# Performance work log

Hardware: AMD Instinct MI355X
Metric: run time of the kernel (lower is better)

Reference implementation:

```python
import jax, jax.numpy as jnp
import numpy as np
import math

B, T, D_MODEL, N_HEADS = 2, 2048, 2048, 16
D_HEAD = D_MODEL // N_HEADS
ROPE_THETA = 10000.0


def setup_inputs() -> dict:
    key = jax.random.key(0)
    ks = jax.random.split(key, 4)
    x = jax.random.normal(ks[0], (B, T, D_MODEL), dtype=jnp.float32)
    # causal mask: True = masked (matches torch masked_fill semantics)
    mask = jnp.triu(jnp.ones((T, T), dtype=bool), k=1)[None, None]  # [1,1,T,T]
    # rotary freqs: complex freqs_cis = exp(i * t * theta^(-2j/d)) -> cos/sin parts
    inv_freq = 1.0 / (ROPE_THETA ** (jnp.arange(0, D_HEAD, 2, dtype=jnp.float32) / D_HEAD))
    angles = jnp.arange(T, dtype=jnp.float32)[:, None] * inv_freq[None, :]  # [T, D_HEAD//2]
    freqs_cos = jnp.cos(angles)
    freqs_sin = jnp.sin(angles)
    s = 1.0 / math.sqrt(D_MODEL)
    Wqkv = jax.random.normal(ks[1], (D_MODEL, 3 * D_MODEL), dtype=jnp.float32) * s
    bqkv = jnp.zeros((3 * D_MODEL,), dtype=jnp.float32)
    Wproj = jax.random.normal(ks[2], (D_MODEL, D_MODEL), dtype=jnp.float32) * s
    bproj = jnp.zeros((D_MODEL,), dtype=jnp.float32)
    return {"x": x, "mask": mask, "freqs_cos": freqs_cos, "freqs_sin": freqs_sin,
            "Wqkv": Wqkv, "bqkv": bqkv, "Wproj": Wproj, "bproj": bproj}


def _rope(t, cos, sin):
    # t: [B,H,T,D]; cos/sin: [1,1,T,D//2]. Complex multiply on (even, odd) pairs.
    t2 = t.reshape(*t.shape[:-1], -1, 2)
    t_re, t_im = t2[..., 0], t2[..., 1]
    out_re = t_re * cos - t_im * sin
    out_im = t_re * sin + t_im * cos
    return jnp.stack([out_re, out_im], axis=-1).reshape(t.shape)


def reference(x, mask, freqs_cos, freqs_sin, Wqkv, bqkv, Wproj, bproj):
    Bb, Tt, C = x.shape
    qkv = x @ Wqkv + bqkv                                   # [B,T,3C]
    q, k, v = jnp.split(qkv, 3, axis=-1)
    def heads(t):
        return t.reshape(Bb, Tt, N_HEADS, D_HEAD).transpose(0, 2, 1, 3)  # [B,H,T,D]
    q, k, v = heads(q), heads(k), heads(v)
    cos = freqs_cos[None, None]                              # [1,1,T,D//2]
    sin = freqs_sin[None, None]
    q = _rope(q, cos, sin)
    k = _rope(k, cos, sin)
    att = jnp.einsum('bhqd,bhkd->bhqk', q, k) / math.sqrt(D_HEAD)
    att = jnp.where(mask, -jnp.inf, att)
    att = jax.nn.softmax(att, axis=-1)
    # attn_dropout is identity in eval mode
    out = jnp.einsum('bhqk,bhkd->bhqd', att, v)              # [B,H,T,D]
    out = out.transpose(0, 2, 1, 3).reshape(Bb, Tt, C)
    return (out @ Wproj + bproj, k, v)
```

## Files before the change

kernel.cpp:

```cpp
#include <hip/hip_runtime.h>
#include <hip/hip_bf16.h>

#define T_SEQ 2048
#define DM    2048
#define NH    16
#define DH    128
#define NBH   32
#define MROWS 4096

typedef __bf16 bf16x8 __attribute__((ext_vector_type(8)));
typedef __bf16 bf16x4 __attribute__((ext_vector_type(4)));
typedef float  f32x4  __attribute__((ext_vector_type(4)));

#define MFMA16 __builtin_amdgcn_mfma_f32_16x16x32_bf16

__device__ __forceinline__ void async_copy16(const void* g, void* l) {
  __builtin_amdgcn_global_load_lds((const __attribute__((address_space(1))) void*)g,
                                   (__attribute__((address_space(3))) void*)l, 16, 0, 0);
}


__global__ void cast_bf16_k(const float* __restrict__ x, __bf16* __restrict__ xb) {
  int i = (blockIdx.x * 256 + threadIdx.x) * 4;
  float4 v = *reinterpret_cast<const float4*>(x + i);
  bf16x4 o;
  o[0] = (__bf16)v.x; o[1] = (__bf16)v.y; o[2] = (__bf16)v.z; o[3] = (__bf16)v.w;
  *reinterpret_cast<bf16x4*>(xb + i) = o;
}

__global__ void transpose_cast_w2(const float* __restrict__ Wqkv, __bf16* __restrict__ WqkvT,
                                  const float* __restrict__ Wproj, __bf16* __restrict__ WprojT) {
  __shared__ float tile[32][33];
  const int bx = (int)blockIdx.x;
  const float* W; __bf16* WT; int N, n0;
  if (bx < 192) { W = Wqkv;  WT = WqkvT;  N = 6144; n0 = bx * 32; }
  else          { W = Wproj; WT = WprojT; N = 2048; n0 = (bx - 192) * 32; }
  const int K = 2048;
  int k0 = blockIdx.y * 32;
  int tx = threadIdx.x, ty = threadIdx.y;
  #pragma unroll
  for (int i = 0; i < 4; i++)
    tile[ty + i * 8][tx] = W[(size_t)(k0 + ty + i * 8) * N + n0 + tx];
  __syncthreads();
  #pragma unroll
  for (int i = 0; i < 4; i++)
    WT[(size_t)(n0 + ty + i * 8) * K + k0 + tx] = (__bf16)tile[tx][ty + i * 8];
}

__global__ void transpose_v(const __bf16* __restrict__ Vb, __bf16* __restrict__ Vtb) {
  __shared__ __bf16 tile[32][34];
  int t0 = blockIdx.x * 32, d0 = blockIdx.y * 32, bh = blockIdx.z;
  const __bf16* src = Vb + (size_t)bh * T_SEQ * DH;
  __bf16* dst = Vtb + (size_t)bh * DH * T_SEQ;
  int tx = threadIdx.x, ty = threadIdx.y;
  #pragma unroll
  for (int i = 0; i < 4; i++)
    tile[ty + i * 8][tx] = src[(size_t)(t0 + ty + i * 8) * DH + d0 + tx];
  __syncthreads();
  #pragma unroll
  for (int i = 0; i < 4; i++)
    dst[(size_t)(d0 + ty + i * 8) * T_SEQ + t0 + tx] = tile[tx][ty + i * 8];
}


__device__ __forceinline__ bf16x8 rds(const __bf16* base, int row, int chunk) {
  return *reinterpret_cast<const bf16x8*>(
      reinterpret_cast<const char*>(base) + row * 128 + ((chunk ^ (row & 7)) << 4));
}

__device__ __forceinline__ void stage64(const __bf16* g, int K, int kt, char* lds,
                                        int wave, int lane) {
  #pragma unroll
  for (int j = 0; j < 4; j++) {
    int r = wave * 32 + j * 8 + (lane >> 3);
    int c = lane & 7;
    const char* src = (const char*)g + (size_t)r * (K * 2) + kt * 128 + ((c ^ (r & 7)) << 4);
    async_copy16(src, lds + wave * 4096 + j * 1024);
  }
}

template <int EPI>
__global__ __launch_bounds__(256, 2) void gemm_bt(
    const __bf16* __restrict__ A, const __bf16* __restrict__ Bt, int K,
    const float* __restrict__ bias,
    const float* __restrict__ fcos, const float* __restrict__ fsin,
    __bf16* __restrict__ Qb, __bf16* __restrict__ Kb, __bf16* __restrict__ Vb,
    float* __restrict__ kout, float* __restrict__ vout,
    float* __restrict__ outp) {
  __shared__ __align__(16) char smem[65536];
  const int tid = threadIdx.x, lane = tid & 63, wave = tid >> 6;
  const int hi = lane >> 4, lo = lane & 15;
  const int wm = (wave >> 1) * 64, wn = (wave & 1) * 64;
  const __bf16* Ab = A + (size_t)blockIdx.y * 128 * K;
  const __bf16* Bb = Bt + (size_t)blockIdx.x * 128 * K;
  f32x4 acc[4][4] = {};
  const int NK = K >> 6;

  stage64(Ab, K, 0, smem, wave, lane);
  stage64(Bb, K, 0, smem + 32768, wave, lane);
  __syncthreads();

  for (int t = 0; t < NK; ++t) {
    const int sel = (t & 1) ? 16384 : 0;
    const __bf16* Ac = (const __bf16*)(smem + sel);
    const __bf16* Bc = (const __bf16*)(smem + 32768 + sel);
    if (t + 1 < NK) {
      stage64(Ab, K, t + 1, smem + (sel ^ 16384), wave, lane);
      stage64(Bb, K, t + 1, smem + 32768 + (sel ^ 16384), wave, lane);
    }
    bf16x8 a0[4], b0[4], a1[4], b1[4];
    #pragma unroll
    for (int m = 0; m < 4; ++m) a0[m] = rds(Ac, wm + m * 16 + lo, hi);
    #pragma unroll
    for (int n = 0; n < 4; ++n) b0[n] = rds(Bc, wn + n * 16 + lo, hi);
    __builtin_amdgcn_s_setprio(1);
    #pragma unroll
    for (int m = 0; m < 4; ++m)
      #pragma unroll
      for (int n = 0; n < 4; ++n)
        acc[m][n] = MFMA16(a0[m], b0[n], acc[m][n], 0, 0, 0);
    __builtin_amdgcn_s_setprio(0);
    #pragma unroll
    for (int m = 0; m < 4; ++m) a1[m] = rds(Ac, wm + m * 16 + lo, 4 + hi);
    #pragma unroll
    for (int n = 0; n < 4; ++n) b1[n] = rds(Bc, wn + n * 16 + lo, 4 + hi);
    __builtin_amdgcn_s_setprio(1);
    #pragma unroll
    for (int m = 0; m < 4; ++m)
      #pragma unroll
      for (int n = 0; n < 4; ++n)
        acc[m][n] = MFMA16(a1[m], b1[n], acc[m][n], 0, 0, 0);
    __builtin_amdgcn_s_setprio(0);
    __syncthreads();
  }

  float* sc = (float*)smem;
  const int rl_r = tid >> 3;
  const int cb   = (tid & 7) * 16;
  #pragma unroll
  for (int cc = 0; cc < 4; ++cc) {
    __syncthreads();
    if ((wave >> 1) == (cc >> 1)) {
      #pragma unroll
      for (int mm = 0; mm < 2; ++mm) {
        int m = (cc & 1) * 2 + mm;
        #pragma unroll
        for (int j = 0; j < 4; ++j) {
          int col = wn + j * 16 + lo;
          int rl = mm * 16 + hi * 4;
          #pragma unroll
          for (int r = 0; r < 4; ++r)
            sc[(rl + r) * 132 + col] = acc[m][j][r];
        }
      }
    }
    __syncthreads();
    float v[16];
    #pragma unroll
    for (int q = 0; q < 4; ++q)
      *reinterpret_cast<float4*>(&v[q * 4]) =
          *reinterpret_cast<const float4*>(&sc[rl_r * 132 + cb + q * 4]);
    const int row = blockIdx.y * 128 + cc * 32 + rl_r;
    const int n0  = blockIdx.x * 128 + cb;
    #pragma unroll
    for (int q = 0; q < 4; ++q) {
      float4 bv = *reinterpret_cast<const float4*>(&bias[n0 + q * 4]);
      v[q * 4 + 0] += bv.x; v[q * 4 + 1] += bv.y;
      v[q * 4 + 2] += bv.z; v[q * 4 + 3] += bv.w;
    }
    if (EPI == 1) {
      const int which = n0 >> 11;
      const int wn2 = n0 & 2047, h = wn2 >> 7, d0 = wn2 & 127;
      const int b = row >> 11, tt = row & 2047;
      if (which < 2) {
        const float* cp = fcos + tt * 64 + (d0 >> 1);
        const float* sp = fsin + tt * 64 + (d0 >> 1);
        float4 c0 = *reinterpret_cast<const float4*>(cp);
        float4 c1 = *reinterpret_cast<const float4*>(cp + 4);
        float4 s0 = *reinterpret_cast<const float4*>(sp);
        float4 s1 = *reinterpret_cast<const float4*>(sp + 4);
        float cs[8] = {c0.x, c0.y, c0.z, c0.w, c1.x, c1.y, c1.z, c1.w};
        float sn[8] = {s0.x, s0.y, s0.z, s0.w, s1.x, s1.y, s1.z, s1.w};
        #pragma unroll
        for (int p = 0; p < 8; ++p) {
          float re = v[2 * p], im = v[2 * p + 1];
          v[2 * p]     = re * cs[p] - im * sn[p];
          v[2 * p + 1] = re * sn[p] + im * cs[p];
        }
      }
      size_t base = (((size_t)(b * NH + h)) * T_SEQ + tt) * DH + d0;
      bf16x8 o0, o1;
      #pragma unroll
      for (int p = 0; p < 8; ++p) { o0[p] = (__bf16)v[p]; o1[p] = (__bf16)v[8 + p]; }
      if (which == 0) {
        *reinterpret_cast<bf16x8*>(Qb + base) = o0;
        *reinterpret_cast<bf16x8*>(Qb + base + 8) = o1;
      } else if (which == 1) {
        *reinterpret_cast<bf16x8*>(Kb + base) = o0;
        *reinterpret_cast<bf16x8*>(Kb + base + 8) = o1;
        #pragma unroll
        for (int q = 0; q < 4; ++q)
          *reinterpret_cast<float4*>(kout + base + q * 4) =
              *reinterpret_cast<const float4*>(&v[q * 4]);
      } else {
        *reinterpret_cast<bf16x8*>(Vb + base) = o0;
        *reinterpret_cast<bf16x8*>(Vb + base + 8) = o1;
        #pragma unroll
        for (int q = 0; q < 4; ++q)
          *reinterpret_cast<float4*>(vout + base + q * 4) =
              *reinterpret_cast<const float4*>(&v[q * 4]);
      }
    } else {
      float* op = outp + (size_t)row * DM + n0;
      #pragma unroll
      for (int q = 0; q < 4; ++q)
        *reinterpret_cast<float4*>(op + q * 4) =
            *reinterpret_cast<const float4*>(&v[q * 4]);
    }
  }
}


__device__ __forceinline__ bf16x8 lds_frag(const __bf16* base, int row, int chunk) {
  return *reinterpret_cast<const bf16x8*>(
      reinterpret_cast<const char*>(base) + row * 256 + ((chunk ^ (row & 7)) << 4));
}

__device__ __forceinline__ void ldK(const __bf16* Kg, int kt, int wave, int lane,
                                    bf16x8 k[4]) {
  const char* g = (const char*)(Kg + (size_t)kt * 64 * DH);
  #pragma unroll
  for (int j = 0; j < 4; j++) {
    int off = j * 4096 + wave * 1024;
    int r = (off >> 8) + (lane >> 4);
    int c = lane & 15;
    k[j] = *reinterpret_cast<const bf16x8*>(g + (size_t)r * 256 + ((c ^ (r & 7)) << 4));
  }
}

__device__ __forceinline__ void ldV(const __bf16* Vg, int kt, int wave, int lane,
                                    bf16x8 v[4]) {
  const char* g = (const char*)Vg;
  const int colB = kt * 128;
  #pragma unroll
  for (int j = 0; j < 4; j++) {
    int off = j * 4096 + wave * 1024;
    int r = (off >> 7) + (lane >> 3);
    int c = lane & 7;
    v[j] = *reinterpret_cast<const bf16x8*>(g + (size_t)r * (T_SEQ * 2) + colB + ((c ^ (r & 7)) << 4));
  }
}

__device__ __forceinline__ void commitKV(__bf16* Ks, __bf16* Vts, int wave, int lane,
                                         const bf16x8 k[4], const bf16x8 v[4]) {
  #pragma unroll
  for (int j = 0; j < 4; j++)
    *reinterpret_cast<bf16x8*>((char*)Ks + j * 4096 + wave * 1024 + lane * 16) = k[j];
  #pragma unroll
  for (int j = 0; j < 4; j++)
    *reinterpret_cast<bf16x8*>((char*)Vts + j * 4096 + wave * 1024 + lane * 16) = v[j];
}

__global__ __launch_bounds__(256, 2) void attn_fwd(
    const __bf16* __restrict__ Qb, const __bf16* __restrict__ Kb,
    const __bf16* __restrict__ Vtb, __bf16* __restrict__ att_out) {
  __shared__ __bf16 Ks[64 * 128];
  __shared__ __bf16 Vts[128 * 64];
  __shared__ __bf16 Ps[4 * 16 * 64];
  const int tid = threadIdx.x, lane = tid & 63, wave = tid >> 6;
  const int hi = lane >> 4, lo = lane & 15;
  const int linear = (int)blockIdx.x;
  const int xcd = linear & 7, rest = linear >> 3;
  const int bh = xcd + 8 * (rest >> 4);
  const int pair = rest & 15;
  const int b = bh >> 4, h = bh & 15;
  const __bf16* Qg = Qb + (size_t)bh * T_SEQ * DH;
  const __bf16* Kg = Kb + (size_t)bh * T_SEQ * DH;
  const __bf16* Vg = Vtb + (size_t)bh * DH * T_SEQ;
  const float scale = 0.08838834764831845f;
  const float L2E = 1.4426950408889634f;
  __bf16* Pw = Ps + wave * 1024;

  for (int pass = 0; pass < 2; ++pass) {
    const int qj = pass ? (31 - pair) : pair;
    const int q0 = qj * 64;
    const int qg = q0 + wave * 16 + lo;
    bf16x8 qf[4];
    const __bf16* qp = Qg + (size_t)qg * DH + hi * 8;
    #pragma unroll
    for (int ks = 0; ks < 4; ++ks) qf[ks] = *reinterpret_cast<const bf16x8*>(qp + ks * 32);
    f32x4 oacc[8] = {};
    float m = -3e38f, l = 0.f;
    const int NT = qj + 1;

    bf16x8 kst[4], vst[4];
    ldK(Kg, 0, wave, lane, kst);
    ldV(Vg, 0, wave, lane, vst);

    for (int kt = 0; kt < NT; ++kt) {
      __syncthreads();
      commitKV(Ks, Vts, wave, lane, kst, vst);
      __syncthreads();
      if (kt + 1 < NT) {
        ldK(Kg, kt + 1, wave, lane, kst);
        ldV(Vg, kt + 1, wave, lane, vst);
      }

      f32x4 sacc[4] = {};
      __builtin_amdgcn_s_setprio(1);
      #pragma unroll
      for (int ks = 0; ks < 4; ++ks)
        #pragma unroll
        for (int sf = 0; sf < 4; ++sf) {
          bf16x8 ak = lds_frag(Ks, sf * 16 + lo, ks * 4 + hi);
          sacc[sf] = MFMA16(ak, qf[ks], sacc[sf], 0, 0, 0);
        }
      __builtin_amdgcn_s_setprio(0);
      const bool diag = (kt == NT - 1);
      float mx = -3e38f;
      #pragma unroll
      for (int sf = 0; sf < 4; ++sf)
        #pragma unroll
        for (int r = 0; r < 4; ++r) {
          float v = sacc[sf][r] * scale;
          if (diag && (kt * 64 + sf * 16 + hi * 4 + r) > qg) v = -3e38f;
          sacc[sf][r] = v;
          mx = fmaxf(mx, v);
        }
      mx = fmaxf(mx, __shfl_xor(mx, 16, 64));
      mx = fmaxf(mx, __shfl_xor(mx, 32, 64));
      const bool nr = __all(mx - m <= 8.0f);
      if (!nr) {
        float mnew = fmaxf(m, mx);
        float alpha = __builtin_exp2f((m - mnew) * L2E);
        m = mnew;
        l *= alpha;
        #pragma unroll
        for (int df = 0; df < 8; ++df) {
          oacc[df][0] *= alpha; oacc[df][1] *= alpha;
          oacc[df][2] *= alpha; oacc[df][3] *= alpha;
        }
      }
      float rs = 0.f;
      #pragma unroll
      for (int sf = 0; sf < 4; ++sf)
        #pragma unroll
        for (int r = 0; r < 4; ++r) {
          float p = __builtin_exp2f((sacc[sf][r] - m) * L2E);
          sacc[sf][r] = p;
          rs += p;
        }
      rs += __shfl_xor(rs, 16, 64);
      rs += __shfl_xor(rs, 32, 64);
      l += rs;
      #pragma unroll
      for (int sf = 0; sf < 4; ++sf) {
        bf16x4 pk;
        pk[0] = (__bf16)sacc[sf][0]; pk[1] = (__bf16)sacc[sf][1];
        pk[2] = (__bf16)sacc[sf][2]; pk[3] = (__bf16)sacc[sf][3];
        int byte = sf * 32 + hi * 8;
        int chunk = byte >> 4, rem = byte & 15;
        char* p = (char*)Pw + lo * 128 + (((chunk ^ (lo & 7)) << 4) | rem);
        *reinterpret_cast<bf16x4*>(p) = pk;
      }
      __builtin_amdgcn_s_setprio(1);
      #pragma unroll
      for (int ks = 0; ks < 2; ++ks) {
        bf16x8 bp = rds(Pw, lo, ks * 4 + hi);
        #pragma unroll
        for (int df = 0; df < 8; ++df) {
          bf16x8 av = rds(Vts, df * 16 + lo, ks * 4 + hi);
          oacc[df] = MFMA16(av, bp, oacc[df], 0, 0, 0);
        }
      }
      __builtin_amdgcn_s_setprio(0);
    }

    float inv = 1.0f / l;
    int qrow = b * T_SEQ + q0 + wave * 16 + lo;
    #pragma unroll
    for (int df = 0; df < 8; ++df) {
      bf16x4 pk;
      pk[0] = (__bf16)(oacc[df][0] * inv);
      pk[1] = (__bf16)(oacc[df][1] * inv);
      pk[2] = (__bf16)(oacc[df][2] * inv);
      pk[3] = (__bf16)(oacc[df][3] * inv);
      int d = df * 16 + hi * 4;
      *reinterpret_cast<bf16x4*>(att_out + (size_t)qrow * DM + h * DH + d) = pk;
    }
  }
}


extern "C" void kernel_launch(void* const* d_in, const int* in_sizes, int n_in,
                              void* d_out, int out_size, void* d_ws, size_t ws_size,
                              hipStream_t stream) {
  const float* x     = (const float*)d_in[0];
  const float* fcos  = (const float*)d_in[2];
  const float* fsin  = (const float*)d_in[3];
  const float* Wqkv  = (const float*)d_in[4];
  const float* bqkv  = (const float*)d_in[5];
  const float* Wproj = (const float*)d_in[6];
  const float* bproj = (const float*)d_in[7];
  float* out  = (float*)d_out;
  float* kout = out + (size_t)8388608;
  float* vout = out + (size_t)16777216;

  char* ws = (char*)d_ws;
  __bf16* xb     = (__bf16*)(ws);
  __bf16* WqkvT  = (__bf16*)(ws + 16777216);
  __bf16* WprojT = (__bf16*)(ws + 41943040);
  __bf16* Qb     = (__bf16*)(ws + 50331648);
  __bf16* Kb     = (__bf16*)(ws + 67108864);
  __bf16* Vb     = (__bf16*)(ws + 83886080);
  __bf16* Vtb    = (__bf16*)(ws + 100663296);
  __bf16* att    = xb;

  cast_bf16_k<<<8192, 256, 0, stream>>>(x, xb);
  transpose_cast_w2<<<dim3(256, 64), dim3(32, 8), 0, stream>>>(Wqkv, WqkvT, Wproj, WprojT);
  gemm_bt<1><<<dim3(48, 32), 256, 0, stream>>>(xb, WqkvT, DM, bqkv, fcos, fsin,
                                               Qb, Kb, Vb, kout, vout, nullptr);
  transpose_v<<<dim3(64, 4, NBH), dim3(32, 8), 0, stream>>>(Vb, Vtb);
  attn_fwd<<<512, 256, 0, stream>>>(Qb, Kb, Vtb, att);
  gemm_bt<0><<<dim3(16, 32), 256, 0, stream>>>(att, WprojT, DM, bproj, nullptr, nullptr,
                                               nullptr, nullptr, nullptr, nullptr, nullptr, out);
}
```

Measured before the change: 278.3 us.

## Double-buffer K/V tiles in attention and fuse prep kernels into one launch

Attention now keeps two LDS buffers for K and V tiles. The next tile is committed after the current compute, so each iteration needs one barrier instead of two. The x cast and weight transpose-cast kernels are merged into a single launch to save launch overhead. This raises LDS use per block, which could limit occupancy.

```diff
diff --git a/kernel.cpp b/kernel.cpp
--- a/kernel.cpp
+++ b/kernel.cpp
@@ -20,24 +20,27 @@
 }
 
 
-__global__ void cast_bf16_k(const float* __restrict__ x, __bf16* __restrict__ xb) {
-  int i = (blockIdx.x * 256 + threadIdx.x) * 4;
-  float4 v = *reinterpret_cast<const float4*>(x + i);
-  bf16x4 o;
-  o[0] = (__bf16)v.x; o[1] = (__bf16)v.y; o[2] = (__bf16)v.z; o[3] = (__bf16)v.w;
-  *reinterpret_cast<bf16x4*>(xb + i) = o;
-}
-
-__global__ void transpose_cast_w2(const float* __restrict__ Wqkv, __bf16* __restrict__ WqkvT,
-                                  const float* __restrict__ Wproj, __bf16* __restrict__ WprojT) {
+__global__ void prep_all(const float* __restrict__ x, __bf16* __restrict__ xb,
+                         const float* __restrict__ Wqkv, __bf16* __restrict__ WqkvT,
+                         const float* __restrict__ Wproj, __bf16* __restrict__ WprojT) {
   __shared__ float tile[32][33];
-  const int bx = (int)blockIdx.x;
+  const int bid = (int)blockIdx.x, tid = threadIdx.x;
+  if (bid < 8192) {
+    int i = (bid * 256 + tid) * 4;
+    float4 v = *reinterpret_cast<const float4*>(x + i);
+    bf16x4 o;
+    o[0] = (__bf16)v.x; o[1] = (__bf16)v.y; o[2] = (__bf16)v.z; o[3] = (__bf16)v.w;
+    *reinterpret_cast<bf16x4*>(xb + i) = o;
+    return;
+  }
+  const int t = bid - 8192;
+  const int bx = t & 255, by = t >> 8;
+  const int tx = tid & 31, ty = tid >> 5;
   const float* W; __bf16* WT; int N, n0;
   if (bx < 192) { W = Wqkv;  WT = WqkvT;  N = 6144; n0 = bx * 32; }
   else          { W = Wproj; WT = WprojT; N = 2048; n0 = (bx - 192) * 32; }
   const int K = 2048;
-  int k0 = blockIdx.y * 32;
-  int tx = threadIdx.x, ty = threadIdx.y;
+  const int k0 = by * 32;
   #pragma unroll
   for (int i = 0; i < 4; i++)
     tile[ty + i * 8][tx] = W[(size_t)(k0 + ty + i * 8) * N + n0 + tx];
@@ -264,8 +267,8 @@
 __global__ __launch_bounds__(256, 2) void attn_fwd(
     const __bf16* __restrict__ Qb, const __bf16* __restrict__ Kb,
     const __bf16* __restrict__ Vtb, __bf16* __restrict__ att_out) {
-  __shared__ __bf16 Ks[64 * 128];
-  __shared__ __bf16 Vts[128 * 64];
+  __shared__ __bf16 Ks[2][64 * 128];
+  __shared__ __bf16 Vts[2][128 * 64];
   __shared__ __bf16 Ps[4 * 16 * 64];
   const int tid = threadIdx.x, lane = tid & 63, wave = tid >> 6;
   const int hi = lane >> 4, lo = lane & 15;
@@ -296,15 +299,14 @@
     bf16x8 kst[4], vst[4];
     ldK(Kg, 0, wave, lane, kst);
     ldV(Vg, 0, wave, lane, vst);
+    __syncthreads();
+    commitKV(Ks[0], Vts[0], wave, lane, kst, vst);
+    __syncthreads();
+    if (1 < NT) { ldK(Kg, 1, wave, lane, kst); ldV(Vg, 1, wave, lane, vst); }
 
     for (int kt = 0; kt < NT; ++kt) {
-      __syncthreads();
-      commitKV(Ks, Vts, wave, lane, kst, vst);
-      __syncthreads();
-      if (kt + 1 < NT) {
-        ldK(Kg, kt + 1, wave, lane, kst);
-        ldV(Vg, kt + 1, wave, lane, vst);
-      }
+      const __bf16* Kc = Ks[kt & 1];
+      const __bf16* Vc = Vts[kt & 1];
 
       f32x4 sacc[4] = {};
       __builtin_amdgcn_s_setprio(1);
@@ -312,7 +314,7 @@
       for (int ks = 0; ks < 4; ++ks)
         #pragma unroll
         for (int sf = 0; sf < 4; ++sf) {
-          bf16x8 ak = lds_frag(Ks, sf * 16 + lo, ks * 4 + hi);
+          bf16x8 ak = lds_frag(Kc, sf * 16 + lo, ks * 4 + hi);
           sacc[sf] = MFMA16(ak, qf[ks], sacc[sf], 0, 0, 0);
         }
       __builtin_amdgcn_s_setprio(0);
@@ -369,11 +371,20 @@
         bf16x8 bp = rds(Pw, lo, ks * 4 + hi);
         #pragma unroll
         for (int df = 0; df < 8; ++df) {
-          bf16x8 av = rds(Vts, df * 16 + lo, ks * 4 + hi);
+          bf16x8 av = rds(Vc, df * 16 + lo, ks * 4 + hi);
           oacc[df] = MFMA16(av, bp, oacc[df], 0, 0, 0);
         }
       }
       __builtin_amdgcn_s_setprio(0);
+
+      if (kt + 1 < NT) {
+        commitKV(Ks[(kt + 1) & 1], Vts[(kt + 1) & 1], wave, lane, kst, vst);
+        __syncthreads();
+        if (kt + 2 < NT) {
+          ldK(Kg, kt + 2, wave, lane, kst);
+          ldV(Vg, kt + 2, wave, lane, vst);
+        }
+      }
     }
 
     float inv = 1.0f / l;
@@ -416,8 +427,7 @@
   __bf16* Vtb    = (__bf16*)(ws + 100663296);
   __bf16* att    = xb;
 
-  cast_bf16_k<<<8192, 256, 0, stream>>>(x, xb);
-  transpose_cast_w2<<<dim3(256, 64), dim3(32, 8), 0, stream>>>(Wqkv, WqkvT, Wproj, WprojT);
+  prep_all<<<24576, 256, 0, stream>>>(x, xb, Wqkv, WqkvT, Wproj, WprojT);
   gemm_bt<1><<<dim3(48, 32), 256, 0, stream>>>(xb, WqkvT, DM, bqkv, fcos, fsin,
                                                Qb, Kb, Vb, kout, vout, nullptr);
   transpose_v<<<dim3(64, 4, NBH), dim3(32, 8), 0, stream>>>(Vb, Vtb);
```

Result: no change. 279.2 us (+0.3%).
